# Optimization experiments

Measured on AMD Instinct MI355X. Metric: run time of the kernel, lower is better.

Reference implementation:

```python
import jax, jax.numpy as jnp
import numpy as np

NEAR, FAR = 0.0, 6.0
N_COARSE, N_IMP = 128, 64
W = 256


def _sdf_net(p, params):
    w0, b0, w1, b1, w2, b2, w3, b3 = params
    h = jax.nn.softplus(p @ w0 + b0)
    h = jax.nn.softplus(h @ w1 + b1)
    h = jax.nn.softplus(h @ w2 + b2)
    out = h @ w3 + b3  # [..., 1 + W]
    return out[..., 0], out[..., 1:]


def _laplace_cdf(x, beta):
    # CDF of zero-mean Laplace with scale beta (VolSDF density)
    return jnp.where(x <= 0, 0.5 * jnp.exp(x / beta), 1.0 - 0.5 * jnp.exp(-x / beta))


def _sample_pdf(bins, weights, n_samples):
    # bins [R, Nc], weights [R, Nc-1] -> [R, n_samples] (deterministic, perturb=False)
    w = weights + 1e-5
    pdf = w / jnp.sum(w, -1, keepdims=True)
    cdf = jnp.concatenate([jnp.zeros_like(pdf[..., :1]), jnp.cumsum(pdf, -1)], -1)  # [R, Nc]
    u = jnp.linspace(0.0, 1.0, n_samples, dtype=bins.dtype)
    u = jnp.broadcast_to(u, (*bins.shape[:-1], n_samples))
    inds = jax.vmap(jnp.searchsorted)(cdf, u)
    below = jnp.clip(inds - 1, 0, cdf.shape[-1] - 1)
    above = jnp.clip(inds, 0, cdf.shape[-1] - 1)
    cdf_b = jnp.take_along_axis(cdf, below, -1)
    cdf_a = jnp.take_along_axis(cdf, above, -1)
    bin_b = jnp.take_along_axis(bins, below, -1)
    bin_a = jnp.take_along_axis(bins, above, -1)
    denom = jnp.where(cdf_a - cdf_b < 1e-5, 1.0, cdf_a - cdf_b)
    t = (u - cdf_b) / denom
    return bin_b + t * (bin_a - bin_b)


def _transmittance_weights(sigma, deltas):
    a = 1.0 - jnp.exp(-sigma * deltas)
    T = jnp.cumprod(jnp.concatenate([jnp.ones_like(a[..., :1]), 1.0 - a + 1e-10], -1), -1)[..., :-1]
    return a * T


def _render(rays_o, rays_d, alpha, beta, sdf_params, rad_params):
    rays_d = rays_d / jnp.linalg.norm(rays_d, axis=-1, keepdims=True)
    R = rays_o.shape[0]
    a_net = alpha[0]
    b_net = beta[0]
    t = jnp.linspace(0.0, 1.0, N_COARSE, dtype=rays_o.dtype)
    d_coarse = jnp.broadcast_to(NEAR * (1.0 - t) + FAR * t, (R, N_COARSE))

    # --- hierarchical fine sampling (torch.no_grad() in source -> stop_gradient) ---
    pts_c = rays_o[:, None, :] + rays_d[:, None, :] * d_coarse[..., None]
    sdf_c, _ = _sdf_net(pts_c, sdf_params)
    sigma_c = a_net * _laplace_cdf(-sdf_c, b_net)
    deltas_c = jnp.diff(d_coarse, axis=-1)
    w_c = _transmittance_weights(sigma_c[..., :-1], deltas_c)
    d_fine = jax.lax.stop_gradient(_sample_pdf(d_coarse, w_c, N_IMP))

    d_all = jnp.sort(jnp.concatenate([d_coarse, d_fine], -1), -1)  # [R, Nc+Nf]
    pts = rays_o[:, None, :] + rays_d[:, None, :] * d_all[..., None]

    sdf, feat = _sdf_net(pts, sdf_params)
    # analytic surface normals: nabla_p sdf(p)
    grad_fn = jax.grad(lambda p: _sdf_net(p, sdf_params)[0])
    nablas = jax.vmap(grad_fn)(pts.reshape(-1, 3)).reshape(pts.shape)
    normals = nablas / (jnp.linalg.norm(nablas, axis=-1, keepdims=True) + 1e-7)

    vdirs = jnp.broadcast_to(rays_d[:, None, :], pts.shape)
    w0, b0, w1, b1, w2, b2 = rad_params
    h = jnp.concatenate([pts, vdirs, normals, feat], -1)  # [R, Nt, 265]
    h = jax.nn.relu(h @ w0 + b0)
    h = jax.nn.relu(h @ w1 + b1)
    rgb = jax.nn.sigmoid(h @ w2 + b2)  # [R, Nt, 3]

    sigma = a_net * _laplace_cdf(-sdf, b_net)
    deltas = jnp.concatenate([jnp.diff(d_all, axis=-1), jnp.full_like(d_all[..., :1], 1e10)], -1)
    weights = _transmittance_weights(sigma, deltas)  # [R, Nt]
    rgb_map = jnp.sum(weights[..., None] * rgb, axis=-2)  # [R, 3]
    return rgb_map


def setup_inputs() -> dict:
    key = jax.random.key(0)
    ks = jax.random.split(key, 16)
    R = 2048

    def w(k, shape):
        return (jax.random.normal(k, shape, dtype=jnp.float32) / np.sqrt(shape[0])).astype(jnp.float32)

    return {
        'rays_o': jax.random.normal(ks[0], (R, 3), dtype=jnp.float32),
        'rays_d': jax.random.normal(ks[1], (R, 3), dtype=jnp.float32),
        'alpha': jnp.ones((1,), dtype=jnp.float32),
        'beta': jnp.ones((1,), dtype=jnp.float32),
        'sdf_w0': w(ks[2], (3, W)), 'sdf_b0': jnp.zeros((W,), jnp.float32),
        'sdf_w1': w(ks[3], (W, W)), 'sdf_b1': jnp.zeros((W,), jnp.float32),
        'sdf_w2': w(ks[4], (W, W)), 'sdf_b2': jnp.zeros((W,), jnp.float32),
        'sdf_w3': w(ks[5], (W, W + 1)), 'sdf_b3': jnp.zeros((W + 1,), jnp.float32),
        'rad_w0': w(ks[6], (9 + W, W)), 'rad_b0': jnp.zeros((W,), jnp.float32),
        'rad_w1': w(ks[7], (W, W)), 'rad_b1': jnp.zeros((W,), jnp.float32),
        'rad_w2': w(ks[8], (W, 3)), 'rad_b2': jnp.zeros((3,), jnp.float32),
    }


def reference(rays_o, rays_d, alpha, beta,
              sdf_w0, sdf_b0, sdf_w1, sdf_b1, sdf_w2, sdf_b2, sdf_w3, sdf_b3,
              rad_w0, rad_b0, rad_w1, rad_b1, rad_w2, rad_b2):
    sdf_params = (sdf_w0, sdf_b0, sdf_w1, sdf_b1, sdf_w2, sdf_b2, sdf_w3, sdf_b3)
    rad_params = (rad_w0, rad_b0, rad_w1, rad_b1, rad_w2, rad_b2)
    return _render(rays_o, rays_d, alpha, beta, sdf_params, rad_params)
```

## Files before the change

### kernel.cpp

```cpp
#include <hip/hip_runtime.h>
#include <math.h>

#define RAYS 2048

typedef unsigned short ushort_t;
typedef short bf16x8 __attribute__((ext_vector_type(8)));
typedef float f32x4 __attribute__((ext_vector_type(4)));

__device__ __forceinline__ float sp_act(float x) {
    return fmaxf(x, 0.0f) + log1pf(expf(-fabsf(x)));
}
__device__ __forceinline__ float lap_cdf(float x, float beta) {
    return (x <= 0.0f) ? 0.5f * expf(x / beta) : 1.0f - 0.5f * expf(-x / beta);
}
__device__ __forceinline__ float sigm(float x) { return 1.0f / (1.0f + expf(-x)); }

__device__ __forceinline__ ushort_t f2bf(float x) {
    union { float f; unsigned int u; } c; c.f = x;
    unsigned int u = c.u + 0x7FFF + ((c.u >> 16) & 1);
    return (ushort_t)(u >> 16);
}
__device__ __forceinline__ float bf2f(ushort_t s) {
    union { unsigned int u; float f; } c; c.u = ((unsigned int)s) << 16;
    return c.f;
}
__device__ __forceinline__ void split2(float v, ushort_t& hi, ushort_t& lo) {
    hi = f2bf(v);
    lo = f2bf(v - bf2f(hi));
}
template<int P>
__device__ __forceinline__ int aidx(int p, int n) { return ((n >> 3) * P + p) * 16 + (n & 7); }

__device__ __forceinline__ void mfma16x16x32(f32x4& c, bf16x8 a, bf16x8 b) {
    asm("v_mfma_f32_16x16x32_bf16 %0, %1, %2, %0" : "+v"(c) : "v"(a), "v"(b));
}

template<int MODE, int KSTEPS, bool BIAS, int PM, bool SPLIT>
__device__ __forceinline__ void mfma_gemm(const ushort_t* __restrict__ A,
                                          const ushort_t* __restrict__ Bp,
                                          const float* __restrict__ bias,
                                          ushort_t* __restrict__ OUT)
{
    constexpr int P = PM * 16;
    const int t = threadIdx.x;
    const int wave = t >> 6, lane = t & 63;
    const int r16 = lane & 15, kg = lane >> 4;
    f32x4 acc[PM][4];
#pragma unroll
    for (int m = 0; m < PM; ++m)
#pragma unroll
        for (int nf = 0; nf < 4; ++nf) acc[m][nf] = 0.0f;

#pragma unroll
    for (int ks = 0; ks < KSTEPS; ++ks) {
        bf16x8 ah[PM], al[PM], bh[4], bl[4];
#pragma unroll
        for (int m = 0; m < PM; ++m) {
            const int ab = ((ks * 4 + kg) * P + m * 16 + r16) * 16;
            ah[m] = *(const bf16x8*)(A + ab);
            if (SPLIT) al[m] = *(const bf16x8*)(A + ab + 8);
        }
#pragma unroll
        for (int nf = 0; nf < 4; ++nf) {
            const int n = wave * 64 + nf * 16 + r16;
            if (SPLIT) {
                const int bb = ((ks * 256 + n) * 4 + kg) * 16;
                bh[nf] = *(const bf16x8*)(Bp + bb);
                bl[nf] = *(const bf16x8*)(Bp + bb + 8);
            } else {
                const int bb = ((ks * 256 + n) * 4 + kg) * 8;
                bh[nf] = *(const bf16x8*)(Bp + bb);
            }
        }
#pragma unroll
        for (int m = 0; m < PM; ++m)
#pragma unroll
            for (int nf = 0; nf < 4; ++nf) {
                mfma16x16x32(acc[m][nf], ah[m], bh[nf]);
                if (SPLIT) {
                    mfma16x16x32(acc[m][nf], ah[m], bl[nf]);
                    mfma16x16x32(acc[m][nf], al[m], bh[nf]);
                }
            }
    }
#pragma unroll
    for (int nf = 0; nf < 4; ++nf) {
        const int n = wave * 64 + nf * 16 + r16;
        float bv = 0.0f;
        if (BIAS) bv = bias[n];
#pragma unroll
        for (int m = 0; m < PM; ++m) {
#pragma unroll
            for (int r = 0; r < 4; ++r) {
                const int p = m * 16 + kg * 4 + r;
                float v = acc[m][nf][r] + bv;
                if (MODE == 1) v = sp_act(v);
                if (MODE == 2) v = fmaxf(v, 0.0f);
                ushort_t hi, lo;
                split2(v, hi, lo);
                const int ob = aidx<P>(p, n);
                OUT[ob] = hi; OUT[ob + 8] = lo;
            }
        }
    }
}

__global__ __launch_bounds__(256) void prep_kernel(
    const float* __restrict__ w1, const float* __restrict__ w2, const float* __restrict__ w3,
    const float* __restrict__ rw0, const float* __restrict__ rw1,
    ushort_t* __restrict__ pw1T, ushort_t* __restrict__ pw2T, ushort_t* __restrict__ pw3T,
    ushort_t* __restrict__ pw2B, ushort_t* __restrict__ pw1B,
    ushort_t* __restrict__ pwR1, ushort_t* __restrict__ pwR0,
    float* __restrict__ w3c0)
{
    const int k = blockIdx.x, mat = blockIdx.y, n = threadIdx.x;
    const int K = (mat == 6) ? 288 : 256;
    if (k >= K) return;
    float v = 0.0f; ushort_t* dst = pw1T; bool lite = false;
    switch (mat) {
        case 0: v = w1[k * 256 + n]; dst = pw1T; break;
        case 1: v = w2[k * 256 + n]; dst = pw2T; break;
        case 2: v = w3[k * 257 + 1 + n]; dst = pw3T;
                if (n == 0) w3c0[k] = w3[k * 257];
                break;
        case 3: v = w2[n * 256 + k]; dst = pw2B; lite = true; break;
        case 4: v = w1[n * 256 + k]; dst = pw1B; lite = true; break;
        case 5: v = rw1[k * 256 + n]; dst = pwR1; break;
        case 6: v = (k < 256) ? rw0[(9 + k) * 256 + n]
                  : (k < 265 ? rw0[(k - 256) * 256 + n] : 0.0f);
                dst = pwR0; break;
    }
    if (lite) {
        dst[(((k >> 5) * 256 + n) * 4 + ((k >> 3) & 3)) * 8 + (k & 7)] = f2bf(v);
    } else {
        const int b = (((k >> 5) * 256 + n) * 4 + ((k >> 3) & 3)) * 16 + (k & 7);
        ushort_t hi, lo; split2(v, hi, lo);
        dst[b] = hi; dst[b + 8] = lo;
    }
}

__global__ __launch_bounds__(256, 1) void coarse_kernel(
    const float* __restrict__ rays_o, const float* __restrict__ rays_d,
    const float* __restrict__ w0, const float* __restrict__ b0,
    const float* __restrict__ b1, const float* __restrict__ b2,
    const ushort_t* __restrict__ pw1T, const ushort_t* __restrict__ pw2T,
    const float* __restrict__ w3c0, const float* __restrict__ b3,
    float* __restrict__ sdf_out)
{
    __shared__ ushort_t bufA[32768], bufB[32768];
    __shared__ float geo[64][3];
    __shared__ float red[256];
    const int t = threadIdx.x;
    const int base = blockIdx.x * 64;

    if (t < 64) {
        const int p = t, pg = base + p;
        const int ray = pg >> 7, i = pg & 127;
        float ox = rays_o[ray*3+0], oy = rays_o[ray*3+1], oz = rays_o[ray*3+2];
        float dx = rays_d[ray*3+0], dy = rays_d[ray*3+1], dz = rays_d[ray*3+2];
        float nm = sqrtf(dx*dx + dy*dy + dz*dz);
        dx /= nm; dy /= nm; dz /= nm;
        float dv = 6.0f * ((float)i / 127.0f);
        geo[p][0] = ox + dx * dv; geo[p][1] = oy + dy * dv; geo[p][2] = oz + dz * dv;
    }
    __syncthreads();
    {
        const int n = t;
        float wa = w0[n], wb = w0[256 + n], wc = w0[512 + n], bb = b0[n];
        for (int p = 0; p < 64; ++p) {
            float z = fmaf(geo[p][0], wa, fmaf(geo[p][1], wb, fmaf(geo[p][2], wc, bb)));
            ushort_t hi, lo; split2(sp_act(z), hi, lo);
            const int ob = aidx<64>(p, n);
            bufA[ob] = hi; bufA[ob + 8] = lo;
        }
    }
    __syncthreads();
    mfma_gemm<1, 8, true, 4, true>(bufA, pw1T, b1, bufB); __syncthreads();
    mfma_gemm<1, 8, true, 4, true>(bufB, pw2T, b2, bufA); __syncthreads();
    {
        const int p = t >> 2, nb = t & 3;
        float s = 0.0f;
        for (int k = nb * 64; k < nb * 64 + 64; ++k) {
            const int ob = aidx<64>(p, k);
            s = fmaf(bf2f(bufA[ob]) + bf2f(bufA[ob + 8]), w3c0[k], s);
        }
        red[t] = s;
    }
    __syncthreads();
    if (t < 64) {
        float s = b3[0] + red[t*4] + red[t*4+1] + red[t*4+2] + red[t*4+3];
        sdf_out[base + t] = s;
    }
}

__global__ __launch_bounds__(256) void sample_kernel(
    const float* __restrict__ sdf_c,
    const float* __restrict__ alpha_p, const float* __restrict__ beta_p,
    float* __restrict__ d_all_g)
{
    __shared__ float sig[4][128];
    __shared__ float dc[4][128];
    __shared__ float wbuf[4][127];
    __shared__ float cdf[4][128];
    __shared__ float dfine[4][64];
    __shared__ float dall[4][192];
    const int t = threadIdx.x;
    const int wv = t >> 6, lane = t & 63;
    const int ray = blockIdx.x * 4 + wv;
    const float alpha = alpha_p[0], beta = beta_p[0];

    for (int i = lane; i < 128; i += 64) {
        float s = sdf_c[ray * 128 + i];
        sig[wv][i] = alpha * lap_cdf(-s, beta);
        dc[wv][i] = 6.0f * ((float)i / 127.0f);
    }
    __syncthreads();
    if (lane == 0) {
        float T = 1.0f, S = 0.0f;
        for (int i = 0; i < 127; ++i) {
            float delta = dc[wv][i + 1] - dc[wv][i];
            float a = 1.0f - expf(-sig[wv][i] * delta);
            float w = a * T;
            T *= (1.0f - a + 1e-10f);
            wbuf[wv][i] = w;
            S += (w + 1e-5f);
        }
        float c = 0.0f;
        cdf[wv][0] = 0.0f;
        for (int i = 0; i < 127; ++i) {
            c += (wbuf[wv][i] + 1e-5f) / S;
            cdf[wv][i + 1] = c;
        }
    }
    __syncthreads();
    {
        float u = (float)lane / 63.0f;
        int lo = 0, hi = 128;
        while (lo < hi) { int m = (lo + hi) >> 1; if (cdf[wv][m] < u) lo = m + 1; else hi = m; }
        int below = lo - 1; if (below < 0) below = 0; if (below > 127) below = 127;
        int above = lo; if (above > 127) above = 127;
        float cb = cdf[wv][below], ca = cdf[wv][above];
        float bb = dc[wv][below], ba = dc[wv][above];
        float den = ca - cb; if (den < 1e-5f) den = 1.0f;
        float tt = (u - cb) / den;
        dfine[wv][lane] = bb + tt * (ba - bb);
    }
    __syncthreads();
    {
        float v = dfine[wv][lane];
        int lo = 0, hi = 128;
        while (lo < hi) { int m = (lo + hi) >> 1; if (dc[wv][m] <= v) lo = m + 1; else hi = m; }
        dall[wv][lane + lo] = v;
    }
    for (int i = lane; i < 128; i += 64) {
        float v = dc[wv][i];
        int lo = 0, hi = 64;
        while (lo < hi) { int m = (lo + hi) >> 1; if (dfine[wv][m] < v) lo = m + 1; else hi = m; }
        dall[wv][i + lo] = v;
    }
    __syncthreads();
    for (int i = lane; i < 192; i += 64) d_all_g[ray * 192 + i] = dall[wv][i];
}

__global__ __launch_bounds__(256, 1) void fine_kernel(
    const float* __restrict__ rays_o, const float* __restrict__ rays_d,
    const float* __restrict__ dall_g,
    const float* __restrict__ w0, const float* __restrict__ b0,
    const float* __restrict__ b1, const float* __restrict__ b2, const float* __restrict__ b3,
    const ushort_t* __restrict__ pw1T, const ushort_t* __restrict__ pw2T,
    const ushort_t* __restrict__ pw3T, const ushort_t* __restrict__ pw2B,
    const ushort_t* __restrict__ pw1B,
    const ushort_t* __restrict__ pwR0, const ushort_t* __restrict__ pwR1,
    const float* __restrict__ w3c0,
    const float* __restrict__ rb0, const float* __restrict__ rb1,
    const float* __restrict__ rw2, const float* __restrict__ rb2,
    float* __restrict__ fsdf, float* __restrict__ frgb)
{
    __shared__ ushort_t buf0[16384], buf1[16384], buf2[16384];
    __shared__ ushort_t fbuf[18432];
    __shared__ float geo[32][6];
    __shared__ float red[768];
    const int t = threadIdx.x;
    const int base = blockIdx.x * 32;

    if (t < 32) {
        const int p = t, pg = base + p;
        const int ray = pg / 192, i = pg - ray * 192;
        float ox = rays_o[ray*3+0], oy = rays_o[ray*3+1], oz = rays_o[ray*3+2];
        float dx = rays_d[ray*3+0], dy = rays_d[ray*3+1], dz = rays_d[ray*3+2];
        float nm = sqrtf(dx*dx + dy*dy + dz*dz);
        dx /= nm; dy /= nm; dz /= nm;
        float dv = dall_g[ray * 192 + i];
        float px = ox + dx * dv, py = oy + dy * dv, pz = oz + dz * dv;
        geo[p][0] = px; geo[p][1] = py; geo[p][2] = pz;
        geo[p][3] = dx; geo[p][4] = dy; geo[p][5] = dz;
        ushort_t hi, lo; int ob;
        split2(px, hi, lo); ob = aidx<32>(p, 256); fbuf[ob] = hi; fbuf[ob+8] = lo;
        split2(py, hi, lo); ob = aidx<32>(p, 257); fbuf[ob] = hi; fbuf[ob+8] = lo;
        split2(pz, hi, lo); ob = aidx<32>(p, 258); fbuf[ob] = hi; fbuf[ob+8] = lo;
        split2(dx, hi, lo); ob = aidx<32>(p, 259); fbuf[ob] = hi; fbuf[ob+8] = lo;
        split2(dy, hi, lo); ob = aidx<32>(p, 260); fbuf[ob] = hi; fbuf[ob+8] = lo;
        split2(dz, hi, lo); ob = aidx<32>(p, 261); fbuf[ob] = hi; fbuf[ob+8] = lo;
    }
    for (int idx = t; idx < 32 * 23; idx += 256) {
        int p = idx & 31, k = 265 + (idx >> 5);
        const int ob = aidx<32>(p, k);
        fbuf[ob] = 0; fbuf[ob + 8] = 0;
    }
    __syncthreads();
    {
        const int n = t;
        float wa = w0[n], wb = w0[256 + n], wc = w0[512 + n], bb = b0[n];
        for (int p = 0; p < 32; ++p) {
            float z = fmaf(geo[p][0], wa, fmaf(geo[p][1], wb, fmaf(geo[p][2], wc, bb)));
            ushort_t hi, lo; split2(sp_act(z), hi, lo);
            const int ob = aidx<32>(p, n);
            buf0[ob] = hi; buf0[ob + 8] = lo;
        }
    }
    __syncthreads();
    mfma_gemm<1, 8, true, 2, true>(buf0, pw1T, b1, buf1); __syncthreads();
    mfma_gemm<1, 8, true, 2, true>(buf1, pw2T, b2, buf2); __syncthreads();
    mfma_gemm<0, 8, true, 2, true>(buf2, pw3T, b3 + 1, fbuf); __syncthreads();
    {
        const int p = t >> 3, nb = t & 7;
        float s = 0.0f;
        for (int k = nb * 32; k < nb * 32 + 32; ++k) {
            const int ob = aidx<32>(p, k);
            s = fmaf(bf2f(buf2[ob]) + bf2f(buf2[ob + 8]), w3c0[k], s);
        }
        red[t] = s;
        const int n = t;
        const float wc0 = w3c0[n];
        for (int p2 = 0; p2 < 32; ++p2) {
            const int ob = aidx<32>(p2, n);
            float h = bf2f(buf2[ob]) + bf2f(buf2[ob + 8]);
            ushort_t hi, lo; split2((1.0f - expf(-h)) * wc0, hi, lo);
            buf0[ob] = hi; buf0[ob + 8] = lo;
        }
    }
    __syncthreads();
    if (t < 32) {
        float s = b3[0];
#pragma unroll
        for (int nb = 0; nb < 8; ++nb) s += red[t * 8 + nb];
        fsdf[base + t] = s;
    }
    __syncthreads();
    mfma_gemm<0, 8, false, 2, false>(buf0, pw2B, nullptr, buf2); __syncthreads();
    {
        const int n = t;
        for (int p = 0; p < 32; ++p) {
            const int ob = aidx<32>(p, n);
            float g = bf2f(buf2[ob]) + bf2f(buf2[ob + 8]);
            float h = bf2f(buf1[ob]) + bf2f(buf1[ob + 8]);
            ushort_t hi, lo; split2(g * (1.0f - expf(-h)), hi, lo);
            buf2[ob] = hi; buf2[ob + 8] = lo;
        }
    }
    __syncthreads();
    mfma_gemm<0, 8, false, 2, false>(buf2, pw1B, nullptr, buf0); __syncthreads();
    {
        const int p = t >> 3, nb = t & 7;
        float px = geo[p][0], py = geo[p][1], pz = geo[p][2];
        float pa = 0.f, pb = 0.f, pc = 0.f;
        for (int k = nb * 32; k < nb * 32 + 32; ++k) {
            float wa = w0[k], wb = w0[256+k], wc = w0[512+k];
            float z = fmaf(px, wa, fmaf(py, wb, fmaf(pz, wc, b0[k])));
            float g = bf2f(buf0[aidx<32>(p, k)]) * sigm(z);
            pa = fmaf(wa, g, pa); pb = fmaf(wb, g, pb); pc = fmaf(wc, g, pc);
        }
        red[t * 3 + 0] = pa; red[t * 3 + 1] = pb; red[t * 3 + 2] = pc;
    }
    __syncthreads();
    if (t < 32) {
        const int p = t;
        float nx = 0.f, ny = 0.f, nz = 0.f;
#pragma unroll
        for (int nb = 0; nb < 8; ++nb) {
            nx += red[(p * 8 + nb) * 3 + 0];
            ny += red[(p * 8 + nb) * 3 + 1];
            nz += red[(p * 8 + nb) * 3 + 2];
        }
        float inv = 1.0f / (sqrtf(nx*nx + ny*ny + nz*nz) + 1e-7f);
        ushort_t hi, lo; int ob;
        split2(nx * inv, hi, lo); ob = aidx<32>(p, 262); fbuf[ob] = hi; fbuf[ob+8] = lo;
        split2(ny * inv, hi, lo); ob = aidx<32>(p, 263); fbuf[ob] = hi; fbuf[ob+8] = lo;
        split2(nz * inv, hi, lo); ob = aidx<32>(p, 264); fbuf[ob] = hi; fbuf[ob+8] = lo;
    }
    __syncthreads();
    mfma_gemm<2, 9, true, 2, true>(fbuf, pwR0, rb0, buf1); __syncthreads();
    mfma_gemm<2, 8, true, 2, true>(buf1, pwR1, rb1, buf2); __syncthreads();
    {
        const int p = t >> 3, nb = t & 7;
        float s0 = 0.f, s1 = 0.f, s2 = 0.f;
        for (int k = nb * 32; k < nb * 32 + 32; ++k) {
            const int ob = aidx<32>(p, k);
            float f = bf2f(buf2[ob]) + bf2f(buf2[ob + 8]);
            s0 = fmaf(f, rw2[k*3+0], s0);
            s1 = fmaf(f, rw2[k*3+1], s1);
            s2 = fmaf(f, rw2[k*3+2], s2);
        }
        red[t * 3 + 0] = s0; red[t * 3 + 1] = s1; red[t * 3 + 2] = s2;
    }
    __syncthreads();
    if (t < 32) {
        const int p = t;
        float s0 = rb2[0], s1 = rb2[1], s2 = rb2[2];
#pragma unroll
        for (int nb = 0; nb < 8; ++nb) {
            s0 += red[(p * 8 + nb) * 3 + 0];
            s1 += red[(p * 8 + nb) * 3 + 1];
            s2 += red[(p * 8 + nb) * 3 + 2];
        }
        frgb[(base + p) * 3 + 0] = sigm(s0);
        frgb[(base + p) * 3 + 1] = sigm(s1);
        frgb[(base + p) * 3 + 2] = sigm(s2);
    }
}

__global__ __launch_bounds__(256) void composite_kernel(
    const float* __restrict__ dall_g, const float* __restrict__ fsdf,
    const float* __restrict__ frgb,
    const float* __restrict__ alpha_p, const float* __restrict__ beta_p,
    float* __restrict__ out)
{
    __shared__ float aa[4][192];
    __shared__ float da[4][192];
    const int t = threadIdx.x;
    const int wv = t >> 6, lane = t & 63;
    const int ray = blockIdx.x * 4 + wv;
    const float alpha = alpha_p[0], beta = beta_p[0];

    for (int i = lane; i < 192; i += 64) da[wv][i] = dall_g[ray * 192 + i];
    __syncthreads();
    for (int i = lane; i < 192; i += 64) {
        float s = fsdf[ray * 192 + i];
        float sg = alpha * lap_cdf(-s, beta);
        float delta = (i < 191) ? (da[wv][i + 1] - da[wv][i]) : 1e10f;
        aa[wv][i] = 1.0f - expf(-sg * delta);
    }
    __syncthreads();
    if (lane == 0) {
        float T = 1.0f, r0 = 0.f, r1 = 0.f, r2 = 0.f;
        for (int i = 0; i < 192; ++i) {
            float a = aa[wv][i];
            float w = a * T;
            T *= (1.0f - a + 1e-10f);
            const float* rp = frgb + (ray * 192 + i) * 3;
            r0 = fmaf(w, rp[0], r0);
            r1 = fmaf(w, rp[1], r1);
            r2 = fmaf(w, rp[2], r2);
        }
        out[ray * 3 + 0] = r0; out[ray * 3 + 1] = r1; out[ray * 3 + 2] = r2;
    }
}

extern "C" void kernel_launch(void* const* d_in, const int* in_sizes, int n_in,
                              void* d_out, int out_size, void* d_ws, size_t ws_size,
                              hipStream_t stream) {
    const float* rays_o = (const float*)d_in[0];
    const float* rays_d = (const float*)d_in[1];
    const float* alpha  = (const float*)d_in[2];
    const float* beta   = (const float*)d_in[3];
    const float* sw0 = (const float*)d_in[4];
    const float* sb0 = (const float*)d_in[5];
    const float* sw1 = (const float*)d_in[6];
    const float* sb1 = (const float*)d_in[7];
    const float* sw2 = (const float*)d_in[8];
    const float* sb2 = (const float*)d_in[9];
    const float* sw3 = (const float*)d_in[10];
    const float* sb3 = (const float*)d_in[11];
    const float* rw0 = (const float*)d_in[12];
    const float* rb0 = (const float*)d_in[13];
    const float* rw1 = (const float*)d_in[14];
    const float* rb1 = (const float*)d_in[15];
    const float* rw2 = (const float*)d_in[16];
    const float* rb2 = (const float*)d_in[17];

    ushort_t* wsu = (ushort_t*)d_ws;
    ushort_t* pw1T = wsu;
    ushort_t* pw2T = pw1T + 131072;
    ushort_t* pw3T = pw2T + 131072;
    ushort_t* pwR1 = pw3T + 131072;
    ushort_t* pwR0 = pwR1 + 131072;
    ushort_t* pw2B = pwR0 + 147456;
    ushort_t* pw1B = pw2B + 65536;
    float* wsf = (float*)(pw1B + 65536);
    float* w3c0  = wsf;               wsf += 256;
    float* sdf_c = wsf;               wsf += RAYS * 128;
    float* dall  = wsf;               wsf += RAYS * 192;
    float* fsdf  = wsf;               wsf += RAYS * 192;
    float* frgb  = wsf;               wsf += RAYS * 192 * 3;

    prep_kernel<<<dim3(288, 7), 256, 0, stream>>>(
        sw1, sw2, sw3, rw0, rw1, pw1T, pw2T, pw3T, pw2B, pw1B, pwR1, pwR0, w3c0);
    coarse_kernel<<<RAYS * 128 / 64, 256, 0, stream>>>(
        rays_o, rays_d, sw0, sb0, sb1, sb2, pw1T, pw2T, w3c0, sb3, sdf_c);
    sample_kernel<<<RAYS / 4, 256, 0, stream>>>(sdf_c, alpha, beta, dall);
    fine_kernel<<<RAYS * 192 / 32, 256, 0, stream>>>(
        rays_o, rays_d, dall,
        sw0, sb0, sb1, sb2, sb3,
        pw1T, pw2T, pw3T, pw2B, pw1B, pwR0, pwR1,
        w3c0, rb0, rb1, rw2, rb2,
        fsdf, frgb);
    composite_kernel<<<RAYS / 4, 256, 0, stream>>>(dall, fsdf, frgb, alpha, beta, (float*)d_out);
}
```

Measured before the change: 6.583 ms.

## Replace coarse-pass MFMA split-bf16 GEMMs with FP32 SIMT tiled matmul

The coarse SDF kernel no longer runs split-bf16 MFMA GEMMs on prepacked weights. It now uses a plain FP32 register-tiled matmul that reads the original weights directly from global memory, with 16 points per block instead of 64. Smaller blocks and less LDS raise occupancy and avoid the hi/lo split overhead. In exchange the matrix cores go unused, weights are re-read from global/L2 by four times as many blocks, and the final dot product runs on only 16 threads serially.

New measurement: 6.587 ms. Within noise of the previous version (+0.1%).

```diff
diff --git a/kernel.cpp b/kernel.cpp
--- a/kernel.cpp
+++ b/kernel.cpp
@@ -102,6 +102,60 @@
                 OUT[ob] = hi; OUT[ob + 8] = lo;
             }
         }
+    }
+}
+
+template<int MODE, bool BIAS>
+__device__ __forceinline__ void tile_mm(const float* __restrict__ Wm,
+                                        const float* __restrict__ bias,
+                                        const float* IN, float* OUT)
+{
+    const int t  = threadIdx.x;
+    const int j0 = (t & 63) << 2;
+    const int p0 = (t >> 6) << 2;
+    float acc[4][4];
+#pragma unroll
+    for (int a = 0; a < 4; ++a)
+#pragma unroll
+        for (int b = 0; b < 4; ++b) acc[a][b] = 0.0f;
+
+    for (int k = 0; k < 256; k += 4) {
+        const float4 w0 = *(const float4*)(Wm + (k + 0) * 256 + j0);
+        const float4 w1 = *(const float4*)(Wm + (k + 1) * 256 + j0);
+        const float4 w2 = *(const float4*)(Wm + (k + 2) * 256 + j0);
+        const float4 w3 = *(const float4*)(Wm + (k + 3) * 256 + j0);
+#pragma unroll
+        for (int pp = 0; pp < 4; ++pp) {
+            const float4 av = *(const float4*)(IN + (p0 + pp) * 256 + k);
+            acc[pp][0] = fmaf(av.x, w0.x, acc[pp][0]);
+            acc[pp][1] = fmaf(av.x, w0.y, acc[pp][1]);
+            acc[pp][2] = fmaf(av.x, w0.z, acc[pp][2]);
+            acc[pp][3] = fmaf(av.x, w0.w, acc[pp][3]);
+            acc[pp][0] = fmaf(av.y, w1.x, acc[pp][0]);
+            acc[pp][1] = fmaf(av.y, w1.y, acc[pp][1]);
+            acc[pp][2] = fmaf(av.y, w1.z, acc[pp][2]);
+            acc[pp][3] = fmaf(av.y, w1.w, acc[pp][3]);
+            acc[pp][0] = fmaf(av.z, w2.x, acc[pp][0]);
+            acc[pp][1] = fmaf(av.z, w2.y, acc[pp][1]);
+            acc[pp][2] = fmaf(av.z, w2.z, acc[pp][2]);
+            acc[pp][3] = fmaf(av.z, w2.w, acc[pp][3]);
+            acc[pp][0] = fmaf(av.w, w3.x, acc[pp][0]);
+            acc[pp][1] = fmaf(av.w, w3.y, acc[pp][1]);
+            acc[pp][2] = fmaf(av.w, w3.z, acc[pp][2]);
+            acc[pp][3] = fmaf(av.w, w3.w, acc[pp][3]);
+        }
+    }
+    float bv0 = 0.f, bv1 = 0.f, bv2 = 0.f, bv3 = 0.f;
+    if constexpr (BIAS) { bv0 = bias[j0]; bv1 = bias[j0+1]; bv2 = bias[j0+2]; bv3 = bias[j0+3]; }
+#pragma unroll
+    for (int pp = 0; pp < 4; ++pp) {
+        float r0 = acc[pp][0] + bv0;
+        float r1 = acc[pp][1] + bv1;
+        float r2 = acc[pp][2] + bv2;
+        float r3 = acc[pp][3] + bv3;
+        if constexpr (MODE == 1) { r0 = sp_act(r0); r1 = sp_act(r1); r2 = sp_act(r2); r3 = sp_act(r3); }
+        if constexpr (MODE == 2) { r0 = fmaxf(r0,0.f); r1 = fmaxf(r1,0.f); r2 = fmaxf(r2,0.f); r3 = fmaxf(r3,0.f); }
+        *(float4*)(OUT + (p0 + pp) * 256 + j0) = make_float4(r0, r1, r2, r3);
     }
 }
 
@@ -139,56 +193,45 @@
     }
 }
 
-__global__ __launch_bounds__(256, 1) void coarse_kernel(
+__global__ __launch_bounds__(256) void coarse_kernel(
     const float* __restrict__ rays_o, const float* __restrict__ rays_d,
     const float* __restrict__ w0, const float* __restrict__ b0,
-    const float* __restrict__ b1, const float* __restrict__ b2,
-    const ushort_t* __restrict__ pw1T, const ushort_t* __restrict__ pw2T,
+    const float* __restrict__ w1, const float* __restrict__ b1,
+    const float* __restrict__ w2, const float* __restrict__ b2,
     const float* __restrict__ w3c0, const float* __restrict__ b3,
     float* __restrict__ sdf_out)
 {
-    __shared__ ushort_t bufA[32768], bufB[32768];
-    __shared__ float geo[64][3];
-    __shared__ float red[256];
+    __shared__ float A[16 * 256];
+    __shared__ float B[16 * 256];
+    __shared__ float pts[16][3];
     const int t = threadIdx.x;
-    const int base = blockIdx.x * 64;
-
-    if (t < 64) {
-        const int p = t, pg = base + p;
-        const int ray = pg >> 7, i = pg & 127;
+    const int base = blockIdx.x * 16;
+
+    if (t < 16) {
+        int pg = base + t;
+        int ray = pg >> 7, i = pg & 127;
         float ox = rays_o[ray*3+0], oy = rays_o[ray*3+1], oz = rays_o[ray*3+2];
         float dx = rays_d[ray*3+0], dy = rays_d[ray*3+1], dz = rays_d[ray*3+2];
-        float nm = sqrtf(dx*dx + dy*dy + dz*dz);
-        dx /= nm; dy /= nm; dz /= nm;
+        float n = sqrtf(dx*dx + dy*dy + dz*dz);
+        dx /= n; dy /= n; dz /= n;
         float dv = 6.0f * ((float)i / 127.0f);
-        geo[p][0] = ox + dx * dv; geo[p][1] = oy + dy * dv; geo[p][2] = oz + dz * dv;
-    }
-    __syncthreads();
-    {
-        const int n = t;
-        float wa = w0[n], wb = w0[256 + n], wc = w0[512 + n], bb = b0[n];
-        for (int p = 0; p < 64; ++p) {
-            float z = fmaf(geo[p][0], wa, fmaf(geo[p][1], wb, fmaf(geo[p][2], wc, bb)));
-            ushort_t hi, lo; split2(sp_act(z), hi, lo);
-            const int ob = aidx<64>(p, n);
-            bufA[ob] = hi; bufA[ob + 8] = lo;
-        }
-    }
-    __syncthreads();
-    mfma_gemm<1, 8, true, 4, true>(bufA, pw1T, b1, bufB); __syncthreads();
-    mfma_gemm<1, 8, true, 4, true>(bufB, pw2T, b2, bufA); __syncthreads();
-    {
-        const int p = t >> 2, nb = t & 3;
-        float s = 0.0f;
-        for (int k = nb * 64; k < nb * 64 + 64; ++k) {
-            const int ob = aidx<64>(p, k);
-            s = fmaf(bf2f(bufA[ob]) + bf2f(bufA[ob + 8]), w3c0[k], s);
-        }
-        red[t] = s;
-    }
-    __syncthreads();
-    if (t < 64) {
-        float s = b3[0] + red[t*4] + red[t*4+1] + red[t*4+2] + red[t*4+3];
+        pts[t][0] = ox + dx * dv; pts[t][1] = oy + dy * dv; pts[t][2] = oz + dz * dv;
+    }
+    __syncthreads();
+    {
+        float wa = w0[t], wb = w0[256 + t], wc = w0[512 + t], bb = b0[t];
+#pragma unroll
+        for (int p = 0; p < 16; ++p) {
+            float z = fmaf(pts[p][0], wa, fmaf(pts[p][1], wb, fmaf(pts[p][2], wc, bb)));
+            A[p * 256 + t] = sp_act(z);
+        }
+    }
+    __syncthreads();
+    tile_mm<1, true>(w1, b1, A, B); __syncthreads();
+    tile_mm<1, true>(w2, b2, B, A); __syncthreads();
+    if (t < 16) {
+        float s = b3[0];
+        for (int k = 0; k < 256; ++k) s = fmaf(A[t * 256 + k], w3c0[k], s);
         sdf_out[base + t] = s;
     }
 }
@@ -495,8 +538,8 @@
 
     prep_kernel<<<dim3(288, 7), 256, 0, stream>>>(
         sw1, sw2, sw3, rw0, rw1, pw1T, pw2T, pw3T, pw2B, pw1B, pwR1, pwR0, w3c0);
-    coarse_kernel<<<RAYS * 128 / 64, 256, 0, stream>>>(
-        rays_o, rays_d, sw0, sb0, sb1, sb2, pw1T, pw2T, w3c0, sb3, sdf_c);
+    coarse_kernel<<<RAYS * 128 / 16, 256, 0, stream>>>(
+        rays_o, rays_d, sw0, sb0, sw1, sb1, sw2, sb2, w3c0, sb3, sdf_c);
     sample_kernel<<<RAYS / 4, 256, 0, stream>>>(sdf_c, alpha, beta, dall);
     fine_kernel<<<RAYS * 192 / 32, 256, 0, stream>>>(
         rays_o, rays_d, dall,
```
